# Optimization experiments

Measured on AMD Instinct MI355X. Metric: run time of the kernel, lower is better.

## Reference

```python
import jax, jax.numpy as jnp
import numpy as np

B, S, D, H = 16, 512, 768, 12
DH = D // H


def setup_inputs() -> dict:
    key = jax.random.key(0)
    ks = jax.random.split(key, 12)
    hidden_states = jax.random.normal(ks[0], (B, S, D), dtype=jnp.float32)
    # additive padding mask: 0 for valid, -10000 for padded tail tokens
    lengths = jax.random.randint(ks[1], (B,), S // 2, S + 1)
    pad = (jnp.arange(S)[None, :] >= lengths[:, None]).astype(jnp.float32)
    attention_mask = (pad * -10000.0)[:, None, None, :]  # [B,1,1,S]
    # row-stochastic graph prior over codes
    pr = jax.random.uniform(ks[2], (B, S, S), dtype=jnp.float32)
    prior = pr / jnp.sum(pr, axis=-1, keepdims=True)
    s = 0.02
    params = dict(
        Wq=jax.random.normal(ks[3], (D, D)) * s, bq=jnp.zeros((D,)),
        Wk=jax.random.normal(ks[4], (D, D)) * s, bk=jnp.zeros((D,)),
        Wv=jax.random.normal(ks[5], (D, D)) * s, bv=jnp.zeros((D,)),
        Wg=jax.random.normal(ks[6], (D, 2)) * s, bg=jnp.zeros((2,)),
        Wo=jax.random.normal(ks[7], (D, D)) * s, bo=jnp.zeros((D,)),
        gamma=jnp.ones((D,)), beta=jnp.zeros((D,)),
    )
    return dict(hidden_states=hidden_states, attention_mask=attention_mask,
                prior=prior, **params)


def _layer_norm(x, gamma, beta, eps=1e-5):
    mu = jnp.mean(x, axis=-1, keepdims=True)
    var = jnp.mean(jnp.square(x - mu), axis=-1, keepdims=True)
    return (x - mu) * jax.lax.rsqrt(var + eps) * gamma + beta


def reference(hidden_states, attention_mask, prior,
              Wq, bq, Wk, bk, Wv, bv, Wg, bg, Wo, bo, gamma, beta):
    b, s, d = hidden_states.shape
    # project and split heads: [B,S,H,DH]
    q = (hidden_states @ Wq + bq).reshape(b, s, H, DH)
    k = (hidden_states @ Wk + bk).reshape(b, s, H, DH)
    v = (hidden_states @ Wv + bv).reshape(b, s, H, DH)
    scores = jnp.einsum('bshd,bthd->bhst', q, k) / jnp.sqrt(jnp.float32(DH))
    scores = scores + attention_mask  # broadcast [B,1,1,S]
    probs = jax.nn.softmax(scores, axis=-1)  # [B,H,S,S]
    # gate: avg-pool over valid tokens, softmax(linear/2)
    valid = (attention_mask.squeeze((1, 2)) == 0.0).astype(hidden_states.dtype)  # [B,S]
    denom = jnp.maximum(jnp.sum(valid, axis=1, keepdims=True), 1.0)
    h_pool = jnp.sum(hidden_states * valid[:, :, None], axis=1) / denom  # [B,D]
    gate = jax.nn.softmax((h_pool @ Wg + bg) / 2.0, axis=-1)  # [B,2]
    probs = probs * gate[:, 0, None, None, None] + prior[:, None, :, :] * gate[:, 1, None, None, None]
    ctx = jnp.einsum('bhst,bthd->bshd', probs, v).reshape(b, s, d)
    out = jax.nn.relu(ctx @ Wo + bo)
    out = _layer_norm(out + hidden_states, gamma, beta)
    return out
```

## Files before the change

kernel.cpp:

```cpp
#include <hip/hip_runtime.h>

#define NB_ 16
#define S_ 512
#define D_ 768
#define H_ 12
#define DH_ 64
#define QT_ 64
#define KT_ 128

typedef __attribute__((ext_vector_type(8))) short bf16x8;
typedef __attribute__((ext_vector_type(4))) float f32x4;
typedef unsigned short ushort_t;

__device__ __forceinline__ unsigned short f2bf(float f){
  unsigned int u = __float_as_uint(f);
  u += 0x7fffu + ((u >> 16) & 1u);
  return (unsigned short)(u >> 16);
}
__device__ __forceinline__ float bf2f(unsigned short s){
  return __uint_as_float(((unsigned int)s) << 16);
}
__device__ __forceinline__ unsigned int pack2(float a, float b){
  return (unsigned int)f2bf(a) | ((unsigned int)f2bf(b) << 16);
}
__device__ __forceinline__ void gld16(const ushort_t* g, ushort_t* l){
  __builtin_amdgcn_global_load_lds((const __attribute__((address_space(1))) unsigned int*)g,
                                   (__attribute__((address_space(3))) unsigned int*)l, 16, 0, 0);
}

__global__ __launch_bounds__(256) void k_wtrans(const float* __restrict__ W0, const float* __restrict__ W1,
                                                const float* __restrict__ W2, const float* __restrict__ W3,
                                                ushort_t* __restrict__ dst){
  const float* W = (blockIdx.z == 0) ? W0 : (blockIdx.z == 1) ? W1 : (blockIdx.z == 2) ? W2 : W3;
  ushort_t* o = dst + (size_t)blockIdx.z * D_ * D_;
  __shared__ float t[32][33];
  int j = threadIdx.x & 31, i0 = threadIdx.x >> 5;
  int kb = blockIdx.y * 32, nb = blockIdx.x * 32;
#pragma unroll
  for (int r = 0; r < 4; r++){
    int i = i0 + r * 8;
    t[i][j] = W[(size_t)(kb + i) * D_ + nb + j];
  }
  __syncthreads();
#pragma unroll
  for (int r = 0; r < 4; r++){
    int i = i0 + r * 8;
    o[(size_t)(nb + i) * D_ + kb + j] = f2bf(t[j][i]);
  }
}

__global__ __launch_bounds__(256) void k_bias3(const float* __restrict__ b0, const float* __restrict__ b1,
                                               const float* __restrict__ b2, float* __restrict__ o){
  int i = blockIdx.x * 256 + threadIdx.x;
  if (i < 3 * D_){
    float v = (i < D_) ? b0[i] : (i < 2 * D_) ? b1[i - D_] : b2[i - 2 * D_];
    o[i] = v;
  }
}

__global__ __launch_bounds__(256) void k_prep(const float* __restrict__ hs, const float* __restrict__ mask,
                                              ushort_t* __restrict__ hsb,
                                              float* __restrict__ partial, float* __restrict__ pcnt){
  int chunk = blockIdx.x, b = blockIdx.y, tid = threadIdx.x;
  const float* mrow = mask + b * S_ + chunk * 64;
  const float* base = hs + ((size_t)b * S_ + chunk * 64) * D_;
  ushort_t* obase = hsb + ((size_t)b * S_ + chunk * 64) * D_;
  float a0 = 0.f, a1 = 0.f, a2 = 0.f, cnt = 0.f;
#pragma unroll 2
  for (int s = 0; s < 64; s++){
    const float* r = base + (size_t)s * D_;
    float x0 = r[tid], x1 = r[tid + 256], x2 = r[tid + 512];
    ushort_t* o = obase + (size_t)s * D_;
    o[tid] = f2bf(x0); o[tid + 256] = f2bf(x1); o[tid + 512] = f2bf(x2);
    if (mrow[s] == 0.0f){ a0 += x0; a1 += x1; a2 += x2; cnt += 1.0f; }
  }
  float* o = partial + (size_t)(b * 8 + chunk) * D_;
  o[tid] = a0; o[tid + 256] = a1; o[tid + 512] = a2;
  if (tid == 0) pcnt[b * 8 + chunk] = cnt;
}

__global__ __launch_bounds__(256) void k_pool2(const float* __restrict__ partial, const float* __restrict__ pcnt,
                                               const float* __restrict__ Wg, const float* __restrict__ bg,
                                               float* __restrict__ gate){
  int b = blockIdx.x, tid = threadIdx.x;
  __shared__ float red[256];
  __shared__ float hp[768];
  float a0 = 0.f, a1 = 0.f, a2 = 0.f;
#pragma unroll
  for (int c = 0; c < 8; c++){
    const float* p = partial + (size_t)(b * 8 + c) * D_;
    a0 += p[tid]; a1 += p[tid + 256]; a2 += p[tid + 512];
  }
  float denom = 0.f;
#pragma unroll
  for (int c = 0; c < 8; c++) denom += pcnt[b * 8 + c];
  float inv = 1.0f / fmaxf(denom, 1.0f);
  hp[tid] = a0 * inv; hp[tid + 256] = a1 * inv; hp[tid + 512] = a2 * inv;
  __syncthreads();
  float p0 = 0.f, p1 = 0.f;
  for (int d = tid; d < D_; d += 256){ p0 += hp[d] * Wg[d * 2]; p1 += hp[d] * Wg[d * 2 + 1]; }
  red[tid] = p0; __syncthreads();
  for (int o = 128; o > 0; o >>= 1){ if (tid < o) red[tid] += red[tid + o]; __syncthreads(); }
  float z0 = red[0]; __syncthreads();
  red[tid] = p1; __syncthreads();
  for (int o = 128; o > 0; o >>= 1){ if (tid < o) red[tid] += red[tid + o]; __syncthreads(); }
  float z1 = red[0];
  if (tid == 0){
    z0 = (z0 + bg[0]) * 0.5f; z1 = (z1 + bg[1]) * 0.5f;
    float m = fmaxf(z0, z1);
    float e0 = __expf(z0 - m), e1 = __expf(z1 - m);
    float ssum = e0 + e1;
    gate[b * 2] = e0 / ssum; gate[b * 2 + 1] = e1 / ssum;
  }
}

template<int OUTBF16, int RELU, int RESID, int AFP32, int MAP>
__global__ __launch_bounds__(256) void k_gemm_bt(
    const void* __restrict__ Ap, long sA, int lda,
    const ushort_t* __restrict__ Bm, long sB, int ldb,
    void* __restrict__ Cp, long sC, int ldc,
    const float* __restrict__ bias,
    const float* __restrict__ resid, float alpha, int K)
{
  __shared__ ushort_t As[128 * 64];
  __shared__ ushort_t Bs[128 * 64];
  int z, bm, bn;
  if (MAP == 2){ z = blockIdx.x; bm = blockIdx.y; bn = blockIdx.z; }
  else if (MAP == 1){ z = blockIdx.z; bm = blockIdx.x; bn = blockIdx.y; }
  else { z = blockIdx.z; bm = blockIdx.y; bn = blockIdx.x; }
  const ushort_t* Ab = AFP32 ? nullptr : ((const ushort_t*)Ap + (size_t)z * sA);
  const float*    Af = AFP32 ? ((const float*)Ap + (size_t)z * sA) : nullptr;
  const ushort_t* Bb = Bm + (size_t)z * sB;
  const long coff = (long)z * sC;
  const int tid = threadIdx.x;
  const int m0 = bm * 128, n0 = bn * 128;
  const int wid = tid >> 6, lane = tid & 63;
  const int quad = lane >> 4, l16 = lane & 15;
  const int wm = wid >> 1, wn = wid & 1;
  const int sw = l16 & 7;

  f32x4 acc[4][4];
#pragma unroll
  for (int i = 0; i < 4; i++)
#pragma unroll
    for (int j = 0; j < 4; j++) acc[i][j] = (f32x4){0.f, 0.f, 0.f, 0.f};

  for (int k0 = 0; k0 < K; k0 += 64){
#pragma unroll
    for (int c = 0; c < 4; c++){
      int idx = tid + c * 256;
      int row = idx >> 3, p = idx & 7;
      int cg = p ^ (row & 7);
      if (AFP32){
        const float* src = Af + (size_t)(m0 + row) * lda + k0 + cg * 8;
        float4 f0 = *(const float4*)src;
        float4 f1 = *(const float4*)(src + 4);
        uint4 pk;
        pk.x = pack2(f0.x, f0.y);
        pk.y = pack2(f0.z, f0.w);
        pk.z = pack2(f1.x, f1.y);
        pk.w = pack2(f1.z, f1.w);
        *(uint4*)(&As[idx * 8]) = pk;
      } else {
        gld16(Ab + (size_t)(m0 + row) * lda + k0 + cg * 8, &As[idx * 8]);
      }
    }
#pragma unroll
    for (int c = 0; c < 4; c++){
      int idx = tid + c * 256;
      int row = idx >> 3, p = idx & 7;
      int cg = p ^ (row & 7);
      gld16(Bb + (size_t)(n0 + row) * ldb + k0 + cg * 8, &Bs[idx * 8]);
    }
    __syncthreads();
#pragma unroll
    for (int ks = 0; ks < 2; ks++){
      bf16x8 af[4], bfv[4];
#pragma unroll
      for (int mi = 0; mi < 4; mi++){
        int row = wm * 64 + mi * 16 + l16;
        af[mi] = *(const bf16x8*)(&As[(row * 8 + ((ks * 4 + quad) ^ sw)) * 8]);
      }
#pragma unroll
      for (int ni = 0; ni < 4; ni++){
        int row = wn * 64 + ni * 16 + l16;
        bfv[ni] = *(const bf16x8*)(&Bs[(row * 8 + ((ks * 4 + quad) ^ sw)) * 8]);
      }
#pragma unroll
      for (int mi = 0; mi < 4; mi++)
#pragma unroll
        for (int ni = 0; ni < 4; ni++)
          acc[mi][ni] = __builtin_amdgcn_mfma_f32_16x16x32_bf16(af[mi], bfv[ni], acc[mi][ni], 0, 0, 0);
    }
    __syncthreads();
  }

#pragma unroll
  for (int mi = 0; mi < 4; mi++){
#pragma unroll
    for (int ni = 0; ni < 4; ni++){
      int col = n0 + wn * 64 + ni * 16 + l16;
      float bcol = bias ? bias[col] : 0.0f;
#pragma unroll
      for (int r = 0; r < 4; r++){
        int row = m0 + wm * 64 + mi * 16 + quad * 4 + r;
        float v = acc[mi][ni][r] * alpha + bcol;
        if (RELU) v = fmaxf(v, 0.0f);
        if (RESID) v += resid[(size_t)row * ldc + col];
        long idx = coff + (long)row * ldc + col;
        if (OUTBF16) ((ushort_t*)Cp)[idx] = f2bf(v);
        else         ((float*)Cp)[idx] = v;
      }
    }
  }
}

__global__ __launch_bounds__(256) void k_vtrans(const ushort_t* __restrict__ v, int ldv,
                                                ushort_t* __restrict__ vt){
  __shared__ ushort_t t[64][66];
  int st = blockIdx.x * 64; int z = blockIdx.y;
  int b = z / H_, h = z - b * H_;
  int tid = threadIdx.x;
  const ushort_t* src = v + ((size_t)b * S_ + st) * ldv + h * DH_;
#pragma unroll
  for (int rep = 0; rep < 8; rep++){
    int idx = rep * 256 + tid;
    int i = idx >> 5, u = idx & 31;
    unsigned int val = *(const unsigned int*)(src + (size_t)i * ldv + u * 2);
    *(unsigned int*)(&t[i][u * 2]) = val;
  }
  __syncthreads();
  ushort_t* dst = vt + (size_t)z * DH_ * S_ + st;
#pragma unroll
  for (int rep = 0; rep < 8; rep++){
    int idx = rep * 256 + tid;
    int d = idx >> 5, u2 = idx & 31;
    unsigned int val = (unsigned int)t[u2 * 2][d] | ((unsigned int)t[u2 * 2 + 1][d] << 16);
    *(unsigned int*)(dst + (size_t)d * S_ + u2 * 2) = val;
  }
}

__global__ __launch_bounds__(256) void k_flash(
    const ushort_t* __restrict__ qkv,
    const ushort_t* __restrict__ vt,
    const ushort_t* __restrict__ priorctx,
    const float* __restrict__ mask,
    const float* __restrict__ gate,
    ushort_t* __restrict__ ctx)
{
  __shared__ ushort_t Ks[KT_ * 64];
  __shared__ ushort_t Vs[DH_ * 128];
  __shared__ ushort_t Ps[QT_ * 136];
  __shared__ float rs[QT_];
  const int z = blockIdx.x, b = z / H_, h = z - b * H_;
  const int q0 = blockIdx.y * QT_;
  const int tid = threadIdx.x;
  const int wid = tid >> 6, lane = tid & 63, quad = lane >> 4, l16 = lane & 15;

  bf16x8 bq[4][2];
#pragma unroll
  for (int ni = 0; ni < 4; ni++)
#pragma unroll
    for (int ks = 0; ks < 2; ks++)
      bq[ni][ks] = *(const bf16x8*)(qkv + ((size_t)(b * S_ + q0 + ni * 16 + l16)) * 2304
                                    + h * DH_ + ks * 32 + quad * 8);
  if (tid < QT_) rs[tid] = 0.f;

  f32x4 accv[4];
#pragma unroll
  for (int ni = 0; ni < 4; ni++) accv[ni] = (f32x4){0.f, 0.f, 0.f, 0.f};

  for (int t0 = 0; t0 < S_; t0 += KT_){
    if (mask[b * S_ + t0] != 0.0f) break;
#pragma unroll
    for (int c = 0; c < 4; c++){
      int idx = tid + c * 256;
      int row = idx >> 3, p = idx & 7;
      int cg = p ^ (row & 7);
      gld16(qkv + ((size_t)(b * S_ + t0 + row)) * 2304 + D_ + h * DH_ + cg * 8, &Ks[idx * 8]);
    }
#pragma unroll
    for (int c = 0; c < 4; c++){
      int idx = tid + c * 256;
      int row = idx >> 4, p = idx & 15;
      int cg = p ^ (row & 15);
      gld16(vt + (size_t)z * (DH_ * S_) + (size_t)row * S_ + t0 + cg * 8, &Vs[idx * 8]);
    }
    __syncthreads();

    f32x4 accs[2][4];
#pragma unroll
    for (int mi = 0; mi < 2; mi++)
#pragma unroll
      for (int ni = 0; ni < 4; ni++) accs[mi][ni] = (f32x4){0.f, 0.f, 0.f, 0.f};
#pragma unroll
    for (int ks = 0; ks < 2; ks++){
      bf16x8 ak[2];
#pragma unroll
      for (int mi = 0; mi < 2; mi++){
        int row = wid * 32 + mi * 16 + l16;
        ak[mi] = *(const bf16x8*)(&Ks[(row * 8 + ((ks * 4 + quad) ^ (l16 & 7))) * 8]);
      }
#pragma unroll
      for (int mi = 0; mi < 2; mi++)
#pragma unroll
        for (int ni = 0; ni < 4; ni++)
          accs[mi][ni] = __builtin_amdgcn_mfma_f32_16x16x32_bf16(ak[mi], bq[ni][ks], accs[mi][ni], 0, 0, 0);
    }

    float mv[2][4];
#pragma unroll
    for (int mi = 0; mi < 2; mi++)
#pragma unroll
      for (int r = 0; r < 4; r++)
        mv[mi][r] = mask[b * S_ + t0 + wid * 32 + mi * 16 + quad * 4 + r];
    float rowpart[4] = {0.f, 0.f, 0.f, 0.f};
#pragma unroll
    for (int mi = 0; mi < 2; mi++){
#pragma unroll
      for (int ni = 0; ni < 4; ni++){
        float e0 = __expf(accs[mi][ni][0] * 0.125f + mv[mi][0]);
        float e1 = __expf(accs[mi][ni][1] * 0.125f + mv[mi][1]);
        float e2 = __expf(accs[mi][ni][2] * 0.125f + mv[mi][2]);
        float e3 = __expf(accs[mi][ni][3] * 0.125f + mv[mi][3]);
        rowpart[ni] += (e0 + e1) + (e2 + e3);
        uint2 pk;
        pk.x = pack2(e0, e1);
        pk.y = pack2(e2, e3);
        *(uint2*)(&Ps[(ni * 16 + l16) * 136 + wid * 32 + mi * 16 + quad * 4]) = pk;
      }
    }
#pragma unroll
    for (int ni = 0; ni < 4; ni++){
      rowpart[ni] += __shfl_xor(rowpart[ni], 16);
      rowpart[ni] += __shfl_xor(rowpart[ni], 32);
    }
    if (lane < 16){
#pragma unroll
      for (int ni = 0; ni < 4; ni++) atomicAdd(&rs[ni * 16 + l16], rowpart[ni]);
    }
    __syncthreads();

#pragma unroll
    for (int ks = 0; ks < 4; ks++){
      bf16x8 ap = *(const bf16x8*)(&Ps[(wid * 16 + l16) * 136 + ks * 32 + quad * 8]);
#pragma unroll
      for (int ni = 0; ni < 4; ni++){
        bf16x8 bv8 = *(const bf16x8*)(&Vs[((ni * 16 + l16) * 16 + ((ks * 4 + quad) ^ l16)) * 8]);
        accv[ni] = __builtin_amdgcn_mfma_f32_16x16x32_bf16(ap, bv8, accv[ni], 0, 0, 0);
      }
    }
    __syncthreads();
  }

  const float g0 = gate[b * 2], g1 = gate[b * 2 + 1];
#pragma unroll
  for (int ni = 0; ni < 4; ni++){
#pragma unroll
    for (int r = 0; r < 4; r++){
      int q = wid * 16 + quad * 4 + r;
      int dh = ni * 16 + l16;
      float scl = g0 / rs[q];
      size_t idx = ((size_t)(b * S_ + q0 + q)) * D_ + h * DH_ + dh;
      float v = accv[ni][r] * scl + g1 * bf2f(priorctx[idx]);
      ctx[idx] = f2bf(v);
    }
  }
}

__global__ __launch_bounds__(256) void k_ln(float* __restrict__ out, const float* __restrict__ gamma,
                                            const float* __restrict__ beta){
  __shared__ float red[256];
  int row = blockIdx.x, tid = threadIdx.x;
  float* p = out + (size_t)row * D_;
  float x0 = p[tid], x1 = p[tid + 256], x2 = p[tid + 512];
  red[tid] = x0 + x1 + x2; __syncthreads();
  for (int o = 128; o > 0; o >>= 1){ if (tid < o) red[tid] += red[tid + o]; __syncthreads(); }
  float mu = red[0] * (1.0f / 768.0f);
  __syncthreads();
  float d0 = x0 - mu, d1 = x1 - mu, d2 = x2 - mu;
  red[tid] = d0 * d0 + d1 * d1 + d2 * d2; __syncthreads();
  for (int o = 128; o > 0; o >>= 1){ if (tid < o) red[tid] += red[tid + o]; __syncthreads(); }
  float rsv = rsqrtf(red[0] * (1.0f / 768.0f) + 1e-5f);
  p[tid]       = d0 * rsv * gamma[tid]       + beta[tid];
  p[tid + 256] = d1 * rsv * gamma[tid + 256] + beta[tid + 256];
  p[tid + 512] = d2 * rsv * gamma[tid + 512] + beta[tid + 512];
}

extern "C" void kernel_launch(void* const* d_in, const int* in_sizes, int n_in,
                              void* d_out, int out_size, void* d_ws, size_t ws_size,
                              hipStream_t stream){
  const float* hs    = (const float*)d_in[0];
  const float* mask  = (const float*)d_in[1];
  const float* prior = (const float*)d_in[2];
  const float* Wq = (const float*)d_in[3];  const float* bq = (const float*)d_in[4];
  const float* Wk = (const float*)d_in[5];  const float* bk = (const float*)d_in[6];
  const float* Wv = (const float*)d_in[7];  const float* bv = (const float*)d_in[8];
  const float* Wg = (const float*)d_in[9];  const float* bg = (const float*)d_in[10];
  const float* Wo = (const float*)d_in[11]; const float* bo = (const float*)d_in[12];
  const float* gamma = (const float*)d_in[13]; const float* beta = (const float*)d_in[14];
  float* out = (float*)d_out;

  size_t off = 0;
  auto alloc = [&](size_t bytes) -> char* {
    char* p = (char*)d_ws + off;
    off += (bytes + 255) & ~(size_t)255;
    return p;
  };
  const size_t HSD = (size_t)NB_ * S_ * D_;
  ushort_t* hsb     = (ushort_t*)alloc(HSD * 2);
  ushort_t* qkvb    = (ushort_t*)alloc(HSD * 3 * 2);
  ushort_t* vtb     = (ushort_t*)alloc(HSD * 2);
  ushort_t* wt      = (ushort_t*)alloc((size_t)4 * D_ * D_ * 2);
  ushort_t* priorctx= (ushort_t*)alloc(HSD * 2);
  ushort_t* ctx     = (ushort_t*)alloc(HSD * 2);
  float*    bqkv    = (float*)alloc((size_t)3 * D_ * 4);
  float*    gate    = (float*)alloc(256);
  float*    partial = (float*)alloc((size_t)NB_ * 8 * D_ * 4);
  float*    pcnt    = (float*)alloc((size_t)NB_ * 8 * 4);

  k_prep<<<dim3(8, NB_), 256, 0, stream>>>(hs, mask, hsb, partial, pcnt);
  k_wtrans<<<dim3(24, 24, 4), 256, 0, stream>>>(Wq, Wk, Wv, Wo, wt);
  k_bias3<<<dim3(9), 256, 0, stream>>>(bq, bk, bv, bqkv);
  k_pool2<<<dim3(NB_), 256, 0, stream>>>(partial, pcnt, Wg, bg, gate);
  k_gemm_bt<1, 0, 0, 0, 1><<<dim3(64, 18, 1), 256, 0, stream>>>(
      hsb, 0, D_, wt, 0, D_, qkvb, 0, 3 * D_, bqkv, nullptr, 1.0f, D_);
  k_vtrans<<<dim3(S_ / 64, NB_ * H_), 256, 0, stream>>>(qkvb + 2 * D_, 3 * D_, vtb);
  k_gemm_bt<1, 0, 0, 1, 2><<<dim3(16, 4, 6), 256, 0, stream>>>(
      prior, (long)S_ * S_, S_, vtb, (long)H_ * DH_ * S_, S_,
      priorctx, (long)S_ * D_, D_, nullptr, nullptr, 1.0f, S_);
  k_flash<<<dim3(NB_ * H_, S_ / QT_), 256, 0, stream>>>(
      qkvb, vtb, priorctx, mask, gate, ctx);
  k_gemm_bt<0, 1, 1, 0, 1><<<dim3(64, 6, 1), 256, 0, stream>>>(
      ctx, 0, D_, wt + 3 * (size_t)D_ * D_, 0, D_, out, 0, D_, bo, hs, 1.0f, D_);
  k_ln<<<dim3(NB_ * S_), 256, 0, stream>>>(out, gamma, beta);
}
```

Before: 291.6 us.

## Fuse setup kernels and write V transposed directly from QKV GEMM epilogue

```diff
diff --git a/kernel.cpp b/kernel.cpp
--- a/kernel.cpp
+++ b/kernel.cpp
@@ -7,6 +7,7 @@
 #define DH_ 64
 #define QT_ 64
 #define KT_ 128
+#define LDQ_ 1536
 
 typedef __attribute__((ext_vector_type(8))) short bf16x8;
 typedef __attribute__((ext_vector_type(4))) float f32x4;
@@ -28,55 +29,59 @@
                                    (__attribute__((address_space(3))) unsigned int*)l, 16, 0, 0);
 }
 
-__global__ __launch_bounds__(256) void k_wtrans(const float* __restrict__ W0, const float* __restrict__ W1,
-                                                const float* __restrict__ W2, const float* __restrict__ W3,
-                                                ushort_t* __restrict__ dst){
-  const float* W = (blockIdx.z == 0) ? W0 : (blockIdx.z == 1) ? W1 : (blockIdx.z == 2) ? W2 : W3;
-  ushort_t* o = dst + (size_t)blockIdx.z * D_ * D_;
+__global__ __launch_bounds__(256) void k_setup(
+    const float* __restrict__ hs, const float* __restrict__ mask,
+    const float* __restrict__ W0, const float* __restrict__ W1,
+    const float* __restrict__ W2, const float* __restrict__ W3,
+    const float* __restrict__ b0, const float* __restrict__ b1, const float* __restrict__ b2,
+    ushort_t* __restrict__ hsb, ushort_t* __restrict__ wt, float* __restrict__ bqkv,
+    float* __restrict__ partial, float* __restrict__ pcnt)
+{
   __shared__ float t[32][33];
-  int j = threadIdx.x & 31, i0 = threadIdx.x >> 5;
-  int kb = blockIdx.y * 32, nb = blockIdx.x * 32;
-#pragma unroll
-  for (int r = 0; r < 4; r++){
-    int i = i0 + r * 8;
-    t[i][j] = W[(size_t)(kb + i) * D_ + nb + j];
-  }
-  __syncthreads();
-#pragma unroll
-  for (int r = 0; r < 4; r++){
-    int i = i0 + r * 8;
-    o[(size_t)(nb + i) * D_ + kb + j] = f2bf(t[j][i]);
-  }
-}
-
-__global__ __launch_bounds__(256) void k_bias3(const float* __restrict__ b0, const float* __restrict__ b1,
-                                               const float* __restrict__ b2, float* __restrict__ o){
-  int i = blockIdx.x * 256 + threadIdx.x;
-  if (i < 3 * D_){
-    float v = (i < D_) ? b0[i] : (i < 2 * D_) ? b1[i - D_] : b2[i - 2 * D_];
-    o[i] = v;
-  }
-}
-
-__global__ __launch_bounds__(256) void k_prep(const float* __restrict__ hs, const float* __restrict__ mask,
-                                              ushort_t* __restrict__ hsb,
-                                              float* __restrict__ partial, float* __restrict__ pcnt){
-  int chunk = blockIdx.x, b = blockIdx.y, tid = threadIdx.x;
-  const float* mrow = mask + b * S_ + chunk * 64;
-  const float* base = hs + ((size_t)b * S_ + chunk * 64) * D_;
-  ushort_t* obase = hsb + ((size_t)b * S_ + chunk * 64) * D_;
-  float a0 = 0.f, a1 = 0.f, a2 = 0.f, cnt = 0.f;
+  const int bx = blockIdx.x, tid = threadIdx.x;
+  if (bx < 512){
+    int chunk = bx & 31, b = bx >> 5;
+    const float* mrow = mask + b * S_ + chunk * 16;
+    const float* base = hs + ((size_t)b * S_ + chunk * 16) * D_;
+    ushort_t* obase = hsb + ((size_t)b * S_ + chunk * 16) * D_;
+    float a0 = 0.f, a1 = 0.f, a2 = 0.f, cnt = 0.f;
 #pragma unroll 2
-  for (int s = 0; s < 64; s++){
-    const float* r = base + (size_t)s * D_;
-    float x0 = r[tid], x1 = r[tid + 256], x2 = r[tid + 512];
-    ushort_t* o = obase + (size_t)s * D_;
-    o[tid] = f2bf(x0); o[tid + 256] = f2bf(x1); o[tid + 512] = f2bf(x2);
-    if (mrow[s] == 0.0f){ a0 += x0; a1 += x1; a2 += x2; cnt += 1.0f; }
-  }
-  float* o = partial + (size_t)(b * 8 + chunk) * D_;
-  o[tid] = a0; o[tid + 256] = a1; o[tid + 512] = a2;
-  if (tid == 0) pcnt[b * 8 + chunk] = cnt;
+    for (int s = 0; s < 16; s++){
+      const float* r = base + (size_t)s * D_;
+      float x0 = r[tid], x1 = r[tid + 256], x2 = r[tid + 512];
+      ushort_t* o = obase + (size_t)s * D_;
+      o[tid] = f2bf(x0); o[tid + 256] = f2bf(x1); o[tid + 512] = f2bf(x2);
+      if (mrow[s] == 0.0f){ a0 += x0; a1 += x1; a2 += x2; cnt += 1.0f; }
+    }
+    float* o = partial + (size_t)(b * 32 + chunk) * D_;
+    o[tid] = a0; o[tid + 256] = a1; o[tid + 512] = a2;
+    if (tid == 0) pcnt[b * 32 + chunk] = cnt;
+  } else if (bx < 512 + 2304){
+    int idx = bx - 512;
+    int z = idx / 576, rem = idx - z * 576;
+    int ky = rem / 24, nx = rem - ky * 24;
+    const float* W = (z == 0) ? W0 : (z == 1) ? W1 : (z == 2) ? W2 : W3;
+    ushort_t* o = wt + (size_t)z * D_ * D_;
+    int j = tid & 31, i0 = tid >> 5;
+    int kb = ky * 32, nb = nx * 32;
+#pragma unroll
+    for (int r = 0; r < 4; r++){
+      int i = i0 + r * 8;
+      t[i][j] = W[(size_t)(kb + i) * D_ + nb + j];
+    }
+    __syncthreads();
+#pragma unroll
+    for (int r = 0; r < 4; r++){
+      int i = i0 + r * 8;
+      o[(size_t)(nb + i) * D_ + kb + j] = f2bf(t[j][i]);
+    }
+  } else {
+    int i = (bx - 2816) * 256 + tid;
+    if (i < 3 * D_){
+      float v = (i < D_) ? b0[i] : (i < 2 * D_) ? b1[i - D_] : b2[i - 2 * D_];
+      bqkv[i] = v;
+    }
+  }
 }
 
 __global__ __launch_bounds__(256) void k_pool2(const float* __restrict__ partial, const float* __restrict__ pcnt,
@@ -87,13 +92,13 @@
   __shared__ float hp[768];
   float a0 = 0.f, a1 = 0.f, a2 = 0.f;
 #pragma unroll
-  for (int c = 0; c < 8; c++){
-    const float* p = partial + (size_t)(b * 8 + c) * D_;
+  for (int c = 0; c < 32; c++){
+    const float* p = partial + (size_t)(b * 32 + c) * D_;
     a0 += p[tid]; a1 += p[tid + 256]; a2 += p[tid + 512];
   }
   float denom = 0.f;
 #pragma unroll
-  for (int c = 0; c < 8; c++) denom += pcnt[b * 8 + c];
+  for (int c = 0; c < 32; c++) denom += pcnt[b * 32 + c];
   float inv = 1.0f / fmaxf(denom, 1.0f);
   hp[tid] = a0 * inv; hp[tid + 256] = a1 * inv; hp[tid + 512] = a2 * inv;
   __syncthreads();
@@ -114,11 +119,11 @@
   }
 }
 
-template<int OUTBF16, int RELU, int RESID, int AFP32, int MAP>
+template<int OUTBF16, int RELU, int RESID, int AFP32, int MAP, int VSPLIT>
 __global__ __launch_bounds__(256) void k_gemm_bt(
     const void* __restrict__ Ap, long sA, int lda,
     const ushort_t* __restrict__ Bm, long sB, int ldb,
-    void* __restrict__ Cp, long sC, int ldc,
+    void* __restrict__ Cp, long sC, int ldc, void* __restrict__ Cp2,
     const float* __restrict__ bias,
     const float* __restrict__ resid, float alpha, int K)
 {
@@ -195,6 +200,26 @@
     __syncthreads();
   }
 
+  if (VSPLIT && n0 >= 1536){
+    ushort_t* vtp = (ushort_t*)Cp2;
+    const int bb = m0 >> 9;
+#pragma unroll
+    for (int mi = 0; mi < 4; mi++){
+#pragma unroll
+      for (int ni = 0; ni < 4; ni++){
+        int col = n0 + wn * 64 + ni * 16 + l16;
+        float bcol = bias[col];
+        int hh = (col - 1536) >> 6, dh = (col - 1536) & 63;
+        int trow = (m0 & 511) + wm * 64 + mi * 16 + quad * 4;
+        uint2 pk;
+        pk.x = pack2(acc[mi][ni][0] + bcol, acc[mi][ni][1] + bcol);
+        pk.y = pack2(acc[mi][ni][2] + bcol, acc[mi][ni][3] + bcol);
+        *(uint2*)(vtp + ((size_t)(bb * H_ + hh) * DH_ + dh) * S_ + trow) = pk;
+      }
+    }
+    return;
+  }
+
 #pragma unroll
   for (int mi = 0; mi < 4; mi++){
 #pragma unroll
@@ -212,31 +237,6 @@
         else         ((float*)Cp)[idx] = v;
       }
     }
-  }
-}
-
-__global__ __launch_bounds__(256) void k_vtrans(const ushort_t* __restrict__ v, int ldv,
-                                                ushort_t* __restrict__ vt){
-  __shared__ ushort_t t[64][66];
-  int st = blockIdx.x * 64; int z = blockIdx.y;
-  int b = z / H_, h = z - b * H_;
-  int tid = threadIdx.x;
-  const ushort_t* src = v + ((size_t)b * S_ + st) * ldv + h * DH_;
-#pragma unroll
-  for (int rep = 0; rep < 8; rep++){
-    int idx = rep * 256 + tid;
-    int i = idx >> 5, u = idx & 31;
-    unsigned int val = *(const unsigned int*)(src + (size_t)i * ldv + u * 2);
-    *(unsigned int*)(&t[i][u * 2]) = val;
-  }
-  __syncthreads();
-  ushort_t* dst = vt + (size_t)z * DH_ * S_ + st;
-#pragma unroll
-  for (int rep = 0; rep < 8; rep++){
-    int idx = rep * 256 + tid;
-    int d = idx >> 5, u2 = idx & 31;
-    unsigned int val = (unsigned int)t[u2 * 2][d] | ((unsigned int)t[u2 * 2 + 1][d] << 16);
-    *(unsigned int*)(dst + (size_t)d * S_ + u2 * 2) = val;
   }
 }
 
@@ -262,7 +262,7 @@
   for (int ni = 0; ni < 4; ni++)
 #pragma unroll
     for (int ks = 0; ks < 2; ks++)
-      bq[ni][ks] = *(const bf16x8*)(qkv + ((size_t)(b * S_ + q0 + ni * 16 + l16)) * 2304
+      bq[ni][ks] = *(const bf16x8*)(qkv + ((size_t)(b * S_ + q0 + ni * 16 + l16)) * LDQ_
                                     + h * DH_ + ks * 32 + quad * 8);
   if (tid < QT_) rs[tid] = 0.f;
 
@@ -277,7 +277,7 @@
       int idx = tid + c * 256;
       int row = idx >> 3, p = idx & 7;
       int cg = p ^ (row & 7);
-      gld16(qkv + ((size_t)(b * S_ + t0 + row)) * 2304 + D_ + h * DH_ + cg * 8, &Ks[idx * 8]);
+      gld16(qkv + ((size_t)(b * S_ + t0 + row)) * LDQ_ + D_ + h * DH_ + cg * 8, &Ks[idx * 8]);
     }
 #pragma unroll
     for (int c = 0; c < 4; c++){
@@ -409,29 +409,27 @@
   };
   const size_t HSD = (size_t)NB_ * S_ * D_;
   ushort_t* hsb     = (ushort_t*)alloc(HSD * 2);
-  ushort_t* qkvb    = (ushort_t*)alloc(HSD * 3 * 2);
+  ushort_t* qkvb    = (ushort_t*)alloc(HSD * 2 * 2);
   ushort_t* vtb     = (ushort_t*)alloc(HSD * 2);
   ushort_t* wt      = (ushort_t*)alloc((size_t)4 * D_ * D_ * 2);
   ushort_t* priorctx= (ushort_t*)alloc(HSD * 2);
   ushort_t* ctx     = (ushort_t*)alloc(HSD * 2);
   float*    bqkv    = (float*)alloc((size_t)3 * D_ * 4);
   float*    gate    = (float*)alloc(256);
-  float*    partial = (float*)alloc((size_t)NB_ * 8 * D_ * 4);
-  float*    pcnt    = (float*)alloc((size_t)NB_ * 8 * 4);
-
-  k_prep<<<dim3(8, NB_), 256, 0, stream>>>(hs, mask, hsb, partial, pcnt);
-  k_wtrans<<<dim3(24, 24, 4), 256, 0, stream>>>(Wq, Wk, Wv, Wo, wt);
-  k_bias3<<<dim3(9), 256, 0, stream>>>(bq, bk, bv, bqkv);
+  float*    partial = (float*)alloc((size_t)NB_ * 32 * D_ * 4);
+  float*    pcnt    = (float*)alloc((size_t)NB_ * 32 * 4);
+
+  k_setup<<<dim3(2825), 256, 0, stream>>>(hs, mask, Wq, Wk, Wv, Wo, bq, bk, bv,
+                                          hsb, wt, bqkv, partial, pcnt);
   k_pool2<<<dim3(NB_), 256, 0, stream>>>(partial, pcnt, Wg, bg, gate);
-  k_gemm_bt<1, 0, 0, 0, 1><<<dim3(64, 18, 1), 256, 0, stream>>>(
-      hsb, 0, D_, wt, 0, D_, qkvb, 0, 3 * D_, bqkv, nullptr, 1.0f, D_);
-  k_vtrans<<<dim3(S_ / 64, NB_ * H_), 256, 0, stream>>>(qkvb + 2 * D_, 3 * D_, vtb);
-  k_gemm_bt<1, 0, 0, 1, 2><<<dim3(16, 4, 6), 256, 0, stream>>>(
+  k_gemm_bt<1, 0, 0, 0, 1, 1><<<dim3(64, 18, 1), 256, 0, stream>>>(
+      hsb, 0, D_, wt, 0, D_, qkvb, 0, LDQ_, vtb, bqkv, nullptr, 1.0f, D_);
+  k_gemm_bt<1, 0, 0, 1, 2, 0><<<dim3(16, 4, 6), 256, 0, stream>>>(
       prior, (long)S_ * S_, S_, vtb, (long)H_ * DH_ * S_, S_,
-      priorctx, (long)S_ * D_, D_, nullptr, nullptr, 1.0f, S_);
+      priorctx, (long)S_ * D_, D_, nullptr, nullptr, nullptr, 1.0f, S_);
   k_flash<<<dim3(NB_ * H_, S_ / QT_), 256, 0, stream>>>(
       qkvb, vtb, priorctx, mask, gate, ctx);
-  k_gemm_bt<0, 1, 1, 0, 1><<<dim3(64, 6, 1), 256, 0, stream>>>(
-      ctx, 0, D_, wt + 3 * (size_t)D_ * D_, 0, D_, out, 0, D_, bo, hs, 1.0f, D_);
+  k_gemm_bt<0, 1, 1, 0, 1, 0><<<dim3(64, 6, 1), 256, 0, stream>>>(
+      ctx, 0, D_, wt + 3 * (size_t)D_ * D_, 0, D_, out, 0, D_, nullptr, bo, hs, 1.0f, D_);
   k_ln<<<dim3(NB_ * S_), 256, 0, stream>>>(out, gamma, beta);
 }
```

Result: faster. 274.6 us (-5.8%).
